# Performance work log

Measured on AMD Instinct MI355X. Metric: run time of the kernel, lower is better.

## Reference

```python
import jax, jax.numpy as jnp
import numpy as np

N_NODES = 50000
N_EDGES = 800000
D = 64


def setup_inputs() -> dict:
    key = jax.random.key(0)
    k1, k2, k3, k4, k5, k6, k7 = jax.random.split(key, 7)
    h = jax.random.normal(k1, (N_NODES, D), dtype=jnp.float32)
    x = jax.random.normal(k2, (N_NODES, 3), dtype=jnp.float32)
    edge_index = jax.random.randint(k3, (2, N_EDGES), 0, N_NODES, dtype=jnp.int64)
    # fc_h: Linear(D, D); fc_x: Linear(D, 1). PyTorch default init scale ~1/sqrt(fan_in).
    s = 1.0 / np.sqrt(D)
    W_h = jax.random.uniform(k4, (D, D), minval=-s, maxval=s, dtype=jnp.float32)
    b_h = jax.random.uniform(k5, (D,), minval=-s, maxval=s, dtype=jnp.float32)
    W_x = jax.random.uniform(k6, (D, 1), minval=-s, maxval=s, dtype=jnp.float32)
    b_x = jax.random.uniform(k7, (1,), minval=-s, maxval=s, dtype=jnp.float32)
    return {"h": h, "x": x, "edge_index": edge_index,
            "W_h": W_h, "b_h": b_h, "W_x": W_x, "b_x": b_x}


def reference(h, x, edge_index, W_h, b_h, W_x, b_x):
    row, col = edge_index[0], edge_index[1]
    h_j = h[col]                                   # [E, D] gather
    delta_x = x[row] - x[col]                      # [E, 3]
    m = jax.nn.relu(h_j @ W_h + b_h)               # [E, D]
    agg_h = jax.ops.segment_sum(m, row, num_segments=h.shape[0])
    h_new = h + agg_h
    weight = jax.nn.relu(h_j @ W_x + b_x)          # [E, 1]
    agg_x = jax.ops.segment_sum(delta_x * weight, row, num_segments=x.shape[0])
    x_new = x + agg_x
    return (h_new, x_new)
```

## Files before the change

### kernel.cpp

```cpp
#include <hip/hip_runtime.h>
#include <hip/hip_fp16.h>

#define N_NODES 50000
#define N_EDGES 800000
#define D 64
#define BLOCK 256

#define NBIN 256
#define BINW 196
#define BCAP 3584
#define EPB 4096
#define NBINBLK 196
#define PREBLK 3125
#define NPW 4
#define SUBS 7
#define RNODES 28
#define QCAP 640

__global__ __launch_bounds__(BLOCK) void pre_bin_kernel(
    const float* __restrict__ h, const float* __restrict__ x,
    const int* __restrict__ eidx,
    const float* __restrict__ Wh, const float* __restrict__ bh,
    const float* __restrict__ Wx, const float* __restrict__ bx,
    __half2* __restrict__ M16, float4* __restrict__ px,
    int* __restrict__ bins, int* __restrict__ gcur) {
  const unsigned b = blockIdx.x;

  if (b < NBINBLK) {
    __shared__ int cnt[NBIN], ssc[NBIN], start[NBIN], cur[NBIN], gbase[NBIN];
    __shared__ int stage[EPB];
    const int t = threadIdx.x;
    cnt[t] = 0;
    __syncthreads();
    const int base = (int)b * EPB;
#pragma unroll 4
    for (int k = 0; k < EPB / BLOCK; ++k) {
      int e = base + k * BLOCK + t;
      if (e < N_EDGES) {
        int row = eidx[e];
        if ((unsigned)row < N_NODES) atomicAdd(&cnt[row / BINW], 1);
      }
    }
    __syncthreads();
    ssc[t] = cnt[t];
    __syncthreads();
    for (int off = 1; off < NBIN; off <<= 1) {
      int v = (t >= off) ? ssc[t - off] : 0;
      __syncthreads();
      ssc[t] += v;
      __syncthreads();
    }
    int ex = ssc[t] - cnt[t];
    start[t] = ex;
    cur[t] = ex;
    gbase[t] = cnt[t] ? atomicAdd(&gcur[t], cnt[t]) : 0;
    __syncthreads();
#pragma unroll 4
    for (int k = 0; k < EPB / BLOCK; ++k) {
      int e = base + k * BLOCK + t;
      if (e < N_EDGES) {
        int row = eidx[e];
        int col = eidx[N_EDGES + e];
        if ((unsigned)row < N_NODES && (unsigned)col < N_NODES) {
          int bb = row / BINW;
          int pos = atomicAdd(&cur[bb], 1);
          stage[pos] = (bb << 24) | ((row - bb * BINW) << 16) | col;
        }
      }
    }
    __syncthreads();
    const int total = ssc[NBIN - 1];
    for (int idx = t; idx < total; idx += BLOCK) {
      int e = stage[idx];
      int bb = ((unsigned)e) >> 24;
      int dst = gbase[bb] + (idx - start[bb]);
      if (dst < BCAP) bins[(size_t)bb * BCAP + dst] = e;
    }
    return;
  }

  const int pid = (int)b - NBINBLK;
  const int wave = threadIdx.x >> 6, lane = threadIdx.x & 63;
  float wreg[D];
#pragma unroll
  for (int k = 0; k < D; ++k) wreg[k] = Wh[k * D + lane];
  const float wxl = Wx[lane];
  const float bhl = bh[lane];
  const float bx0 = bx[0];
  const int nbase = pid * (4 * NPW) + wave * NPW;

#pragma unroll 2
  for (int nn = 0; nn < NPW; ++nn) {
    const int i = nbase + nn;
    const int iu = __builtin_amdgcn_readfirstlane(i);
    const float* __restrict__ hr = h + (size_t)iu * D;
    float a0 = bhl, a1 = 0.f, a2 = 0.f, a3 = 0.f;
#pragma unroll
    for (int k = 0; k < D; k += 4) {
      a0 = fmaf(hr[k],     wreg[k],     a0);
      a1 = fmaf(hr[k + 1], wreg[k + 1], a1);
      a2 = fmaf(hr[k + 2], wreg[k + 2], a2);
      a3 = fmaf(hr[k + 3], wreg[k + 3], a3);
    }
    float m = fmaxf((a0 + a1) + (a2 + a3), 0.0f);
    float mn = __shfl_down(m, 1);
    if (!(lane & 1))
      M16[(size_t)iu * 32 + (lane >> 1)] = __floats2half2_rn(m, mn);
    float hl = hr[lane];
    float wx = hl * wxl;
#pragma unroll
    for (int off = 32; off > 0; off >>= 1) wx += __shfl_down(wx, off);
    if (lane == 0) {
      float w = fmaxf(wx + bx0, 0.0f);
      px[iu] = make_float4(w, w * x[(size_t)iu * 3 + 0],
                           w * x[(size_t)iu * 3 + 1],
                           w * x[(size_t)iu * 3 + 2]);
    }
  }
}

__global__ __launch_bounds__(256) void agg_kernel(
    const float* __restrict__ h, const float* __restrict__ x,
    const int* __restrict__ bins, const int* __restrict__ gcur,
    const __half2* __restrict__ M16, const float4* __restrict__ px,
    float* __restrict__ out) {
  __shared__ int qs[QCAP];
  __shared__ int hist[RNODES];
  __shared__ int rstart[RNODES + 1];
  __shared__ int rcur[RNODES];

  const int t = threadIdx.x;
  const int bin = blockIdx.x / SUBS, sub = blockIdx.x % SUBS;
  const int lbase = sub * RNODES;
  const int gb = bin * BINW + lbase;
  const int R = min(RNODES, N_NODES - gb);
  if (R <= 0) return;

  if (t < RNODES) hist[t] = 0;
  __syncthreads();

  const int n = min(gcur[bin], BCAP);
  const int* bs = bins + (size_t)bin * BCAP;
  for (int i = t; i < n; i += 256) {
    int e = bs[i];
    unsigned d = (unsigned)((e >> 16) & 0xff) - (unsigned)lbase;
    if (d < (unsigned)R) atomicAdd(&hist[d], 1);
  }
  __syncthreads();
  if (t < 64) {
    int myh = (t < R) ? hist[t] : 0;
    int v = myh;
#pragma unroll
    for (int off = 1; off < 64; off <<= 1) {
      int u = __shfl_up(v, off);
      if (t >= off) v += u;
    }
    if (t == 0) rstart[0] = 0;
    if (t < R) { rstart[t + 1] = v; rcur[t] = v - myh; }
  }
  __syncthreads();
  for (int i = t; i < n; i += 256) {
    int e = bs[i];
    unsigned d = (unsigned)((e >> 16) & 0xff) - (unsigned)lbase;
    if (d < (unsigned)R) {
      int pos = atomicAdd(&rcur[d], 1);
      if (pos < QCAP) qs[pos] = e;
    }
  }
  __syncthreads();

  const float* pxf = (const float*)px;
  const int hl = t & 31;
  const int stream = ((t >> 6) << 1) | ((t >> 5) & 1);
  const int bl = t & 32;
  const size_t xb = (size_t)N_NODES * D;

  for (int rr = stream; rr < R; rr += 8) {
    int beg = min(rstart[rr], QCAP);
    int end = min(rstart[rr + 1], QCAP);
    float a0 = 0.f, a1 = 0.f, ps = 0.f;
    for (int qi = beg; qi < end; qi += 8) {
      __half2 g[8];
      float pv[8];
      bool val[8];
#pragma unroll
      for (int j = 0; j < 8; ++j) {
        int idx = qi + j;
        val[j] = idx < end;
        int e = qs[val[j] ? idx : beg];
        int c = e & 0xffff;
        pv[j] = 0.f;
        if (val[j]) {
          g[j] = M16[(size_t)c * 32 + hl];
          if (hl < 4) pv[j] = pxf[c * 4 + hl];
        }
      }
#pragma unroll
      for (int j = 0; j < 8; ++j)
        if (val[j]) {
          float2 f = __half22float2(g[j]);
          a0 += f.x; a1 += f.y; ps += pv[j];
        }
    }
    int gn = gb + rr;
    float2 hvv = *(const float2*)(h + (size_t)gn * D + 2 * hl);
    *(float2*)(out + (size_t)gn * D + 2 * hl) =
        make_float2(hvv.x + a0, hvv.y + a1);
    float W = __shfl(ps, bl);
    float pc = __shfl(ps, bl + hl + 1);
    if (hl < 3)
      out[xb + (size_t)gn * 3 + hl] =
          fmaf(x[(size_t)gn * 3 + hl], 1.0f + W, -pc);
  }
}


__global__ __launch_bounds__(256) void init_out_kernel(
    const float* __restrict__ h, const float* __restrict__ x,
    float* __restrict__ out) {
  const int NH4 = N_NODES * D / 4;
  const int NT4 = (N_NODES * D + N_NODES * 3) / 4;
  int i = blockIdx.x * 256 + threadIdx.x;
  if (i >= NT4) return;
  float4 v;
  if (i < NH4) v = ((const float4*)h)[i];
  else         v = ((const float4*)x)[i - NH4];
  ((float4*)out)[i] = v;
}

__global__ __launch_bounds__(256) void edge_kernel(
    const float* __restrict__ h, const float* __restrict__ x,
    const int* __restrict__ eidx,
    const float* __restrict__ Wh, const float* __restrict__ bh,
    const float* __restrict__ Wx, const float* __restrict__ bx,
    float* __restrict__ out) {
  int e = blockIdx.x * 256 + threadIdx.x;
  if (e >= N_EDGES) return;
  int row = eidx[e];
  int col = eidx[N_EDGES + e];
  if ((unsigned)row >= N_NODES || (unsigned)col >= N_NODES) return;
  const float* hj = h + (size_t)col * D;
  float acc[D];
#pragma unroll
  for (int dd = 0; dd < D; ++dd) acc[dd] = bh[dd];
  float wsum = bx[0];
#pragma unroll 2
  for (int kg = 0; kg < D / 4; ++kg) {
    float4 hv = *(const float4*)(hj + kg * 4);
#pragma unroll
    for (int j = 0; j < 4; ++j) {
      float hk = (j == 0) ? hv.x : (j == 1) ? hv.y : (j == 2) ? hv.z : hv.w;
      int k = kg * 4 + j;
      wsum = fmaf(hk, Wx[k], wsum);
      const float* wrow = Wh + k * D;
#pragma unroll
      for (int dd = 0; dd < D; ++dd) acc[dd] = fmaf(hk, wrow[dd], acc[dd]);
    }
  }
  float* outh = out + (size_t)row * D;
#pragma unroll
  for (int dd = 0; dd < D; ++dd) atomicAdd(&outh[dd], fmaxf(acc[dd], 0.0f));
  float w = fmaxf(wsum, 0.0f);
  float* outx = out + (size_t)N_NODES * D + (size_t)row * 3;
  const float* xr = x + (size_t)row * 3;
  const float* xc = x + (size_t)col * 3;
#pragma unroll
  for (int c = 0; c < 3; ++c) atomicAdd(&outx[c], (xr[c] - xc[c]) * w);
}


extern "C" void kernel_launch(void* const* d_in, const int* in_sizes, int n_in,
                              void* d_out, int out_size, void* d_ws, size_t ws_size,
                              hipStream_t stream) {
  const float* h    = (const float*)d_in[0];
  const float* x    = (const float*)d_in[1];
  const int*   eidx = (const int*)d_in[2];
  const float* Wh   = (const float*)d_in[3];
  const float* bh   = (const float*)d_in[4];
  const float* Wx   = (const float*)d_in[5];
  const float* bx   = (const float*)d_in[6];
  float* out = (float*)d_out;

  size_t need = (size_t)N_NODES * D * 2 + (size_t)N_NODES * 16 +
                (size_t)NBIN * BCAP * 4 + 1024;

  if (ws_size < need) {
    const int NT4 = (N_NODES * D + N_NODES * 3) / 4;
    init_out_kernel<<<(NT4 + 255) / 256, 256, 0, stream>>>(h, x, out);
    edge_kernel<<<(N_EDGES + 255) / 256, 256, 0, stream>>>(
        h, x, eidx, Wh, bh, Wx, bx, out);
    return;
  }

  __half2* M16 = (__half2*)d_ws;
  float4*  px  = (float4*)((char*)d_ws + (size_t)N_NODES * D * 2);
  int*     bins = (int*)((char*)px + (size_t)N_NODES * 16);
  int*     gcur = bins + (size_t)NBIN * BCAP;

  hipMemsetAsync(gcur, 0, NBIN * sizeof(int), stream);
  pre_bin_kernel<<<NBINBLK + PREBLK, BLOCK, 0, stream>>>(
      h, x, eidx, Wh, bh, Wx, bx, M16, px, bins, gcur);
  agg_kernel<<<NBIN * SUBS, 256, 0, stream>>>(
      h, x, bins, gcur, M16, px, out);
}
```

Baseline: 127.7 us.

## Use one thread per node for the transform and 16 lanes per node in aggregation

The node transform now gives each thread a whole node. It keeps 64 accumulators in registers, reads h and the weights with float4 loads, and writes the fp16 message row with vector stores, instead of spreading each node over a wave of lanes. The aggregation kernel now handles each destination node with 16 lanes doing 8-byte gathers, so 16 nodes are in flight per block instead of 8. It also uses 4 sub-blocks of 49 nodes per bin with a larger queue. The aim is to cut lane overhead and cross-lane shuffles and to raise gather parallelism. The cost is a higher register count and only 196 blocks for the transform, which may leave many compute units idle.

```diff
diff --git a/kernel.cpp b/kernel.cpp
--- a/kernel.cpp
+++ b/kernel.cpp
@@ -11,11 +11,10 @@
 #define BCAP 3584
 #define EPB 4096
 #define NBINBLK 196
-#define PREBLK 3125
-#define NPW 4
-#define SUBS 7
-#define RNODES 28
-#define QCAP 640
+#define PREBLK 196
+#define SUBS 4
+#define RNODES 49
+#define QCAP 1024
 
 __global__ __launch_bounds__(BLOCK) void pre_bin_kernel(
     const float* __restrict__ h, const float* __restrict__ x,
@@ -80,43 +79,51 @@
   }
 
   const int pid = (int)b - NBINBLK;
-  const int wave = threadIdx.x >> 6, lane = threadIdx.x & 63;
-  float wreg[D];
-#pragma unroll
-  for (int k = 0; k < D; ++k) wreg[k] = Wh[k * D + lane];
-  const float wxl = Wx[lane];
-  const float bhl = bh[lane];
-  const float bx0 = bx[0];
-  const int nbase = pid * (4 * NPW) + wave * NPW;
-
-#pragma unroll 2
-  for (int nn = 0; nn < NPW; ++nn) {
-    const int i = nbase + nn;
-    const int iu = __builtin_amdgcn_readfirstlane(i);
-    const float* __restrict__ hr = h + (size_t)iu * D;
-    float a0 = bhl, a1 = 0.f, a2 = 0.f, a3 = 0.f;
-#pragma unroll
-    for (int k = 0; k < D; k += 4) {
-      a0 = fmaf(hr[k],     wreg[k],     a0);
-      a1 = fmaf(hr[k + 1], wreg[k + 1], a1);
-      a2 = fmaf(hr[k + 2], wreg[k + 2], a2);
-      a3 = fmaf(hr[k + 3], wreg[k + 3], a3);
-    }
-    float m = fmaxf((a0 + a1) + (a2 + a3), 0.0f);
-    float mn = __shfl_down(m, 1);
-    if (!(lane & 1))
-      M16[(size_t)iu * 32 + (lane >> 1)] = __floats2half2_rn(m, mn);
-    float hl = hr[lane];
-    float wx = hl * wxl;
-#pragma unroll
-    for (int off = 32; off > 0; off >>= 1) wx += __shfl_down(wx, off);
-    if (lane == 0) {
-      float w = fmaxf(wx + bx0, 0.0f);
-      px[iu] = make_float4(w, w * x[(size_t)iu * 3 + 0],
-                           w * x[(size_t)iu * 3 + 1],
-                           w * x[(size_t)iu * 3 + 2]);
-    }
-  }
+  const int i = pid * BLOCK + threadIdx.x;
+  if (i >= N_NODES) return;
+
+  const float4* __restrict__ h4 = (const float4*)(h + (size_t)i * D);
+  const float4* __restrict__ Wx4 = (const float4*)Wx;
+
+  float acc[D];
+#pragma unroll
+  for (int d = 0; d < D; ++d) acc[d] = bh[d];
+  float wx = bx[0];
+
+  for (int q = 0; q < D / 4; ++q) {
+    float4 hv = h4[q];
+    float4 wxv = Wx4[q];
+    wx = fmaf(hv.x, wxv.x, fmaf(hv.y, wxv.y, fmaf(hv.z, wxv.z,
+         fmaf(hv.w, wxv.w, wx))));
+#pragma unroll
+    for (int r = 0; r < 4; ++r) {
+      float hk = (r == 0) ? hv.x : (r == 1) ? hv.y : (r == 2) ? hv.z : hv.w;
+      const float4* wr4 = (const float4*)(Wh + (q * 4 + r) * D);
+#pragma unroll
+      for (int dq = 0; dq < D / 4; ++dq) {
+        float4 wv = wr4[dq];
+        acc[4 * dq + 0] = fmaf(hk, wv.x, acc[4 * dq + 0]);
+        acc[4 * dq + 1] = fmaf(hk, wv.y, acc[4 * dq + 1]);
+        acc[4 * dq + 2] = fmaf(hk, wv.z, acc[4 * dq + 2]);
+        acc[4 * dq + 3] = fmaf(hk, wv.w, acc[4 * dq + 3]);
+      }
+    }
+  }
+
+  __half2 hh[D / 2];
+#pragma unroll
+  for (int j = 0; j < D / 2; ++j)
+    hh[j] = __floats2half2_rn(fmaxf(acc[2 * j], 0.0f),
+                              fmaxf(acc[2 * j + 1], 0.0f));
+  float4* mrow = (float4*)(M16 + (size_t)i * 32);
+  const float4* hhp = (const float4*)hh;
+#pragma unroll
+  for (int q = 0; q < 8; ++q) mrow[q] = hhp[q];
+
+  float w = fmaxf(wx, 0.0f);
+  px[i] = make_float4(w, w * x[(size_t)i * 3 + 0],
+                      w * x[(size_t)i * 3 + 1],
+                      w * x[(size_t)i * 3 + 2]);
 }
 
 __global__ __launch_bounds__(256) void agg_kernel(
@@ -130,7 +137,7 @@
   __shared__ int rcur[RNODES];
 
   const int t = threadIdx.x;
-  const int bin = blockIdx.x / SUBS, sub = blockIdx.x % SUBS;
+  const int bin = blockIdx.x >> 2, sub = blockIdx.x & 3;
   const int lbase = sub * RNODES;
   const int gb = bin * BINW + lbase;
   const int R = min(RNODES, N_NODES - gb);
@@ -143,8 +150,8 @@
   const int* bs = bins + (size_t)bin * BCAP;
   for (int i = t; i < n; i += 256) {
     int e = bs[i];
-    unsigned d = (unsigned)((e >> 16) & 0xff) - (unsigned)lbase;
-    if (d < (unsigned)R) atomicAdd(&hist[d], 1);
+    unsigned dd = (unsigned)((e >> 16) & 0xff) - (unsigned)lbase;
+    if (dd < (unsigned)R) atomicAdd(&hist[dd], 1);
   }
   __syncthreads();
   if (t < 64) {
@@ -161,26 +168,27 @@
   __syncthreads();
   for (int i = t; i < n; i += 256) {
     int e = bs[i];
-    unsigned d = (unsigned)((e >> 16) & 0xff) - (unsigned)lbase;
-    if (d < (unsigned)R) {
-      int pos = atomicAdd(&rcur[d], 1);
+    unsigned dd = (unsigned)((e >> 16) & 0xff) - (unsigned)lbase;
+    if (dd < (unsigned)R) {
+      int pos = atomicAdd(&rcur[dd], 1);
       if (pos < QCAP) qs[pos] = e;
     }
   }
   __syncthreads();
 
   const float* pxf = (const float*)px;
-  const int hl = t & 31;
-  const int stream = ((t >> 6) << 1) | ((t >> 5) & 1);
-  const int bl = t & 32;
+  const float2* M2 = (const float2*)M16;
+  const int l16 = t & 15;
+  const int stream = t >> 4;
+  const int wbase = t & 48;
   const size_t xb = (size_t)N_NODES * D;
 
-  for (int rr = stream; rr < R; rr += 8) {
+  for (int rr = stream; rr < R; rr += 16) {
     int beg = min(rstart[rr], QCAP);
     int end = min(rstart[rr + 1], QCAP);
-    float a0 = 0.f, a1 = 0.f, ps = 0.f;
+    float a0 = 0.f, a1 = 0.f, a2 = 0.f, a3 = 0.f, ps = 0.f;
     for (int qi = beg; qi < end; qi += 8) {
-      __half2 g[8];
+      float2 g[8];
       float pv[8];
       bool val[8];
 #pragma unroll
@@ -191,26 +199,29 @@
         int c = e & 0xffff;
         pv[j] = 0.f;
         if (val[j]) {
-          g[j] = M16[(size_t)c * 32 + hl];
-          if (hl < 4) pv[j] = pxf[c * 4 + hl];
+          g[j] = M2[(size_t)c * 16 + l16];
+          if (l16 < 4) pv[j] = pxf[c * 4 + l16];
         }
       }
 #pragma unroll
       for (int j = 0; j < 8; ++j)
         if (val[j]) {
-          float2 f = __half22float2(g[j]);
-          a0 += f.x; a1 += f.y; ps += pv[j];
+          const __half2* hp = (const __half2*)&g[j];
+          float2 f0 = __half22float2(hp[0]);
+          float2 f1 = __half22float2(hp[1]);
+          a0 += f0.x; a1 += f0.y; a2 += f1.x; a3 += f1.y;
+          ps += pv[j];
         }
     }
     int gn = gb + rr;
-    float2 hvv = *(const float2*)(h + (size_t)gn * D + 2 * hl);
-    *(float2*)(out + (size_t)gn * D + 2 * hl) =
-        make_float2(hvv.x + a0, hvv.y + a1);
-    float W = __shfl(ps, bl);
-    float pc = __shfl(ps, bl + hl + 1);
-    if (hl < 3)
-      out[xb + (size_t)gn * 3 + hl] =
-          fmaf(x[(size_t)gn * 3 + hl], 1.0f + W, -pc);
+    float4 hvv = ((const float4*)h)[(size_t)gn * 16 + l16];
+    ((float4*)out)[(size_t)gn * 16 + l16] =
+        make_float4(hvv.x + a0, hvv.y + a1, hvv.z + a2, hvv.w + a3);
+    float W = __shfl(ps, wbase);
+    float pc = __shfl(ps, wbase + l16 + 1);
+    if (l16 < 3)
+      out[xb + (size_t)gn * 3 + l16] =
+          fmaf(x[(size_t)gn * 3 + l16], 1.0f + W, -pc);
   }
 }
 
```

Result: no change. 128.6 us (+0.7%).
